# Optimization experiments

Hardware: AMD Instinct MI355X
Metric: run time of the kernel (lower is better)

The kernel has to match this reference:

```python
import jax, jax.numpy as jnp
import numpy as np

B, N, C = 4, 1370, 1024
H, DH = 16, C // 16
N_ROPE = 1369  # patch tokens covered by RoPE (prefix=1 CLS token)


def _rotate_half(x):
    x1, x2 = jnp.split(x, 2, axis=-1)
    return jnp.concatenate([-x2, x1], axis=-1)


def _rope_apply(x, sin, cos):
    return x * cos + _rotate_half(x) * sin


def setup_inputs() -> dict:
    key = jax.random.key(0)
    ks = jax.random.split(key, 7)
    return {
        "x": jax.random.normal(ks[0], (B, N, C), dtype=jnp.float32),
        "sin": jax.random.normal(ks[1], (N_ROPE, DH), dtype=jnp.float32),
        "cos": jax.random.normal(ks[2], (N_ROPE, DH), dtype=jnp.float32),
        "w_qkv": jax.random.normal(ks[3], (C, 3 * C), dtype=jnp.float32) * (C ** -0.5),
        "b_qkv": jax.random.normal(ks[4], (3 * C,), dtype=jnp.float32) * 0.02,
        "w_proj": jax.random.normal(ks[5], (C, C), dtype=jnp.float32) * (C ** -0.5),
        "b_proj": jax.random.normal(ks[6], (C,), dtype=jnp.float32) * 0.02,
    }


def reference(x, sin, cos, w_qkv, b_qkv, w_proj, b_proj):
    b, n, c = x.shape
    # QKV projection -> [3, B, H, N, DH]
    qkv = (x @ w_qkv + b_qkv).reshape(b, n, 3, H, DH).transpose(2, 0, 3, 1, 4)
    q, k, v = qkv[0], qkv[1], qkv[2]
    # RoPE on the last N_ROPE tokens (prefix tokens, e.g. CLS, left untouched)
    prefix = n - sin.shape[-2]
    q = jnp.concatenate([q[:, :, :prefix, :], _rope_apply(q[:, :, prefix:, :], sin, cos)], axis=-2)
    k = jnp.concatenate([k[:, :, :prefix, :], _rope_apply(k[:, :, prefix:, :], sin, cos)], axis=-2)
    # Full attention
    scale = 1.0 / jnp.sqrt(jnp.asarray(DH, dtype=x.dtype))
    attn = jnp.einsum('bhqd,bhkd->bhqk', q, k) * scale
    attn = jax.nn.softmax(attn, axis=-1)
    out = jnp.einsum('bhqk,bhkd->bhqd', attn, v)
    out = out.transpose(0, 2, 1, 3).reshape(b, n, c)
    return out @ w_proj + b_proj
```

## Files before the change

### kernel.cpp

```cpp
#include <hip/hip_runtime.h>
#include <hip/hip_bf16.h>

#define B_ 4
#define N_ 1370
#define C_ 1024
#define H_ 16
#define DH_ 64
#define NR_ 1369
#define M_ (B_*N_)
#define VTS_ 1408
#define ALS 64
#define PLS 72

#define QSCALE 0.1803368801111f

typedef _Float16 f16x8  __attribute__((ext_vector_type(8)));
typedef __bf16   bf16x8 __attribute__((ext_vector_type(8)));
typedef float    f32x4  __attribute__((ext_vector_type(4)));

__device__ __forceinline__ f16x8 ld_frag_h(const unsigned short* p) {
    uint4 u = *(const uint4*)p;
    return __builtin_bit_cast(f16x8, u);
}
__device__ __forceinline__ bf16x8 ld_frag_b(const unsigned short* p) {
    uint4 u = *(const uint4*)p;
    return __builtin_bit_cast(bf16x8, u);
}
__device__ __forceinline__ unsigned short f2h(float f) {
    _Float16 h = (_Float16)f;
    return __builtin_bit_cast(unsigned short, h);
}
__device__ __forceinline__ unsigned short f2bf(float f) {
    __hip_bfloat16 h = __float2bfloat16(f);
    return __builtin_bit_cast(unsigned short, h);
}
__device__ __forceinline__ bf16x8 ones_bf() {
    uint4 u = make_uint4(0x3F803F80u, 0x3F803F80u, 0x3F803F80u, 0x3F803F80u);
    return __builtin_bit_cast(bf16x8, u);
}

__device__ __forceinline__ void load_lds16(const unsigned short* g, unsigned short* l) {
    __builtin_amdgcn_global_load_lds(
        (const __attribute__((address_space(1))) unsigned int*)g,
        (__attribute__((address_space(3))) unsigned int*)l,
        16, 0, 0);
}

#define XBLK 5480
#define WQBLK 768
#define WPBLK 256
__global__ __launch_bounds__(256)
void prep_k(const float* __restrict__ x, unsigned short* __restrict__ xo,
            const float* __restrict__ wq, unsigned short* __restrict__ wqt,
            const float* __restrict__ wp, unsigned short* __restrict__ wpt)
{
    __shared__ unsigned short Th[64][68];
    int bid = blockIdx.x;
    if (bid < XBLK) {
        const int i = bid * 256 + threadIdx.x;
        float4 v = ((const float4*)x)[i];
        ushort4 h;
        h.x = f2h(v.x); h.y = f2h(v.y); h.z = f2h(v.z); h.w = f2h(v.w);
        ((ushort4*)xo)[i] = h;
        return;
    }
    bid -= XBLK;
    const float* w; unsigned short* wt; int Ncol, nb;
    if (bid < WQBLK) { w = wq; wt = wqt; Ncol = 3072; nb = 48; }
    else { bid -= WQBLK; w = wp; wt = wpt; Ncol = 1024; nb = 16; }
    const int tid = threadIdx.x, tx = tid & 15, ty = tid >> 4;
    const int n0 = (bid % nb) * 64, k0 = (bid / nb) * 64;
    #pragma unroll
    for (int i = 0; i < 4; ++i) {
        const int k = ty + i * 16;
        float4 v = *(const float4*)&w[(size_t)(k0 + k) * Ncol + n0 + tx * 4];
        Th[k][tx*4+0] = f2h(v.x); Th[k][tx*4+1] = f2h(v.y);
        Th[k][tx*4+2] = f2h(v.z); Th[k][tx*4+3] = f2h(v.w);
    }
    __syncthreads();
    #pragma unroll
    for (int i = 0; i < 4; ++i) {
        const int n = ty + i * 16;
        ushort4 o;
        o.x = Th[tx*4+0][n]; o.y = Th[tx*4+1][n]; o.z = Th[tx*4+2][n]; o.w = Th[tx*4+3][n];
        *(ushort4*)&wt[(size_t)(n0 + n) * 1024 + k0 + tx * 4] = o;
    }
}

__global__ __launch_bounds__(256)
void transpose_v_k(const unsigned short* __restrict__ v, unsigned short* __restrict__ vt) {
    __shared__ unsigned short Th[64][68];
    const int tid = threadIdx.x, tx = tid & 15, ty = tid >> 4;
    const int bh = blockIdx.y, t0 = blockIdx.x * 64;
    const unsigned short* vp = v + (size_t)bh * N_ * DH_;
    unsigned short* vtp = vt + (size_t)bh * DH_ * VTS_;
    #pragma unroll
    for (int i = 0; i < 4; ++i) {
        const int tok = ty + i * 16;
        const int gtok = t0 + tok;
        ushort4 val;
        if (gtok < N_) val = *(const ushort4*)&vp[(size_t)gtok * DH_ + tx * 4];
        else { val.x = 0; val.y = 0; val.z = 0; val.w = 0; }
        Th[tok][tx*4+0] = val.x; Th[tok][tx*4+1] = val.y;
        Th[tok][tx*4+2] = val.z; Th[tok][tx*4+3] = val.w;
    }
    __syncthreads();
    #pragma unroll
    for (int i = 0; i < 4; ++i) {
        const int d = ty + i * 16;
        ushort4 o;
        o.x = Th[tx*4+0][d]; o.y = Th[tx*4+1][d]; o.z = Th[tx*4+2][d]; o.w = Th[tx*4+3][d];
        *(ushort4*)&vtp[(size_t)d * VTS_ + t0 + tx * 4] = o;
    }
}

__global__ __launch_bounds__(512, 4)
void gemm_qkv8(const unsigned short* __restrict__ A, const unsigned short* __restrict__ Bt,
               const float* __restrict__ bias,
               unsigned short* __restrict__ qb, unsigned short* __restrict__ kb,
               unsigned short* __restrict__ vb,
               const float* __restrict__ sinp, const float* __restrict__ cosp)
{
    __shared__ __align__(16) unsigned short A_s[2][192 * 64];
    __shared__ __align__(16) unsigned short B_s[2][128 * 64];

    const int tid = threadIdx.x;
    const int wave = tid >> 6, lane = tid & 63;
    const int quad = lane >> 4, l16 = lane & 15;
    const int m0 = blockIdx.y * 192, n0 = blockIdx.x * 128;
    const int mwave = (wave >> 1) * 48;
    const int nwave = (wave & 1) * 64;

    const int srow = lane >> 3;
    const int gseg = (lane & 7) ^ srow;

    f32x4 acc[3][4] = {};

    auto stage = [&](int kc, int buf) {
        const int kof = kc * 64;
        #pragma unroll
        for (int i = 0; i < 3; ++i) {
            const int rbase = wave * 24 + i * 8;
            int arow = m0 + rbase + srow;
            if (arow > M_ - 1) arow = M_ - 1;
            load_lds16(A + (size_t)arow * 1024 + kof + gseg * 8, &A_s[buf][rbase * 64]);
        }
        #pragma unroll
        for (int i = 0; i < 2; ++i) {
            const int rbase = wave * 16 + i * 8;
            const int brow = n0 + rbase + srow;
            load_lds16(Bt + (size_t)brow * 1024 + kof + gseg * 8, &B_s[buf][rbase * 64]);
        }
    };

    stage(0, 0);

    for (int kc = 0; kc < 16; ++kc) {
        const int cur = kc & 1;
        __syncthreads();
        if (kc + 1 < 16) stage(kc + 1, cur ^ 1);

        #pragma unroll
        for (int kh = 0; kh < 2; ++kh) {
            const int soff = (((kh * 4 + quad) ^ (l16 & 7)) << 3);
            f16x8 a[3], b[4];
            #pragma unroll
            for (int t = 0; t < 3; ++t)
                a[t] = ld_frag_h(&A_s[cur][(mwave + t * 16 + l16) * 64 + soff]);
            #pragma unroll
            for (int t = 0; t < 4; ++t)
                b[t] = ld_frag_h(&B_s[cur][(nwave + t * 16 + l16) * 64 + soff]);
            #pragma unroll
            for (int i = 0; i < 3; ++i)
                #pragma unroll
                for (int j = 0; j < 4; ++j)
                    acc[i][j] = __builtin_amdgcn_mfma_f32_16x16x32_f16(a[i], b[j], acc[i][j], 0, 0, 0);
        }
    }

    const int nbase = n0 + nwave;
    const int part = nbase >> 10;
    const int h = (nbase & 1023) >> 6;
    #pragma unroll
    for (int i = 0; i < 3; ++i) {
        #pragma unroll
        for (int r = 0; r < 4; ++r) {
            const int gm = m0 + mwave + i * 16 + quad * 4 + r;
            if (gm >= M_) continue;
            const int b = gm / N_;
            const int tok = gm - b * N_;

            float val[4];
            #pragma unroll
            for (int j = 0; j < 4; ++j)
                val[j] = acc[i][j][r] + bias[nbase + j * 16 + l16];

            if (part < 2 && tok >= 1) {
                const float* sp = sinp + (size_t)(tok - 1) * DH_;
                const float* cp = cosp + (size_t)(tok - 1) * DH_;
                const float s0 = sp[l16],      s1 = sp[16 + l16];
                const float s2 = sp[32 + l16], s3 = sp[48 + l16];
                const float c0 = cp[l16],      c1 = cp[16 + l16];
                const float c2 = cp[32 + l16], c3 = cp[48 + l16];
                const float n0v = fmaf(val[0], c0, -val[2] * s0);
                const float n1v = fmaf(val[1], c1, -val[3] * s1);
                const float n2v = fmaf(val[2], c2,  val[0] * s2);
                const float n3v = fmaf(val[3], c3,  val[1] * s3);
                val[0] = n0v; val[1] = n1v; val[2] = n2v; val[3] = n3v;
            }

            const int bh = b * H_ + h;
            #pragma unroll
            for (int j = 0; j < 4; ++j) {
                const int d = j * 16 + l16;
                if (part == 0)      qb[((size_t)bh * N_ + tok) * DH_ + d] = f2h(val[j] * QSCALE);
                else if (part == 1) kb[((size_t)bh * N_ + tok) * DH_ + d] = f2h(val[j]);
                else                vb[((size_t)bh * N_ + tok) * DH_ + d] = f2bf(val[j]);
            }
        }
    }
}

__global__ __launch_bounds__(256)
void gemm_proj2(const unsigned short* __restrict__ A, const unsigned short* __restrict__ Bt,
                const float* __restrict__ bias, float* __restrict__ out)
{
    __shared__ __align__(16) unsigned short A_s[2][64 * 64];
    __shared__ __align__(16) unsigned short B_s[2][128 * 64];

    const int tid = threadIdx.x;
    const int wave = tid >> 6, lane = tid & 63;
    const int quad = lane >> 4, l16 = lane & 15;
    const int m0 = blockIdx.y * 64, n0 = blockIdx.x * 128;
    const int mwave = (wave & 1) * 32, nwave = (wave >> 1) * 64;

    const int srow = lane >> 3;
    const int gseg = (lane & 7) ^ srow;

    f32x4 acc[2][4] = {};

    auto stage = [&](int kc, int buf) {
        const int kof = kc * 64;
        #pragma unroll
        for (int i = 0; i < 2; ++i) {
            const int rbase = wave * 16 + i * 8;
            int arow = m0 + rbase + srow;
            if (arow > M_ - 1) arow = M_ - 1;
            load_lds16(A + (size_t)arow * 1024 + kof + gseg * 8, &A_s[buf][rbase * 64]);
        }
        #pragma unroll
        for (int i = 0; i < 4; ++i) {
            const int rbase = wave * 32 + i * 8;
            const int brow = n0 + rbase + srow;
            load_lds16(Bt + (size_t)brow * 1024 + kof + gseg * 8, &B_s[buf][rbase * 64]);
        }
    };

    stage(0, 0);

    for (int kc = 0; kc < 16; ++kc) {
        const int cur = kc & 1;
        __syncthreads();
        if (kc + 1 < 16) stage(kc + 1, cur ^ 1);

        #pragma unroll
        for (int kh = 0; kh < 2; ++kh) {
            const int soff = (((kh * 4 + quad) ^ (l16 & 7)) << 3);
            f16x8 a[2], b[4];
            #pragma unroll
            for (int t = 0; t < 2; ++t)
                a[t] = ld_frag_h(&A_s[cur][(mwave + t * 16 + l16) * 64 + soff]);
            #pragma unroll
            for (int t = 0; t < 4; ++t)
                b[t] = ld_frag_h(&B_s[cur][(nwave + t * 16 + l16) * 64 + soff]);
            #pragma unroll
            for (int i = 0; i < 2; ++i)
                #pragma unroll
                for (int j = 0; j < 4; ++j)
                    acc[i][j] = __builtin_amdgcn_mfma_f32_16x16x32_f16(a[i], b[j], acc[i][j], 0, 0, 0);
        }
    }

    #pragma unroll
    for (int i = 0; i < 2; ++i) {
        #pragma unroll
        for (int r = 0; r < 4; ++r) {
            const int gm = m0 + mwave + i * 16 + quad * 4 + r;
            if (gm >= M_) continue;
            #pragma unroll
            for (int j = 0; j < 4; ++j) {
                const int gn = n0 + nwave + j * 16 + l16;
                out[(size_t)gm * 1024 + gn] = acc[i][j][r] + bias[gn];
            }
        }
    }
}

__global__ __launch_bounds__(512, 6)
void attn_k(const unsigned short* __restrict__ q, const unsigned short* __restrict__ k,
            const unsigned short* __restrict__ vt, unsigned short* __restrict__ out)
{
    __shared__ __align__(16) unsigned short Ks[2][64 * ALS];
    __shared__ __align__(16) unsigned short Vs[2][64 * ALS];
    __shared__ __align__(16) unsigned short Ps[8 * 16 * PLS];

    const int tid  = threadIdx.x;
    const int wave = tid >> 6, lane = tid & 63;
    const int quad = lane >> 4, l16 = lane & 15;
    const int srow = lane >> 3;
    const int gseg = (lane & 7) ^ srow;

    const int id  = blockIdx.x;
    const int lid = (id & 7) * 88 + (id >> 3);
    const int bh  = lid / 11;
    const int q0  = (lid - bh * 11) * 128;

    const unsigned short* qp  = q  + (size_t)bh * N_ * DH_;
    const unsigned short* kp  = k  + (size_t)bh * N_ * DH_;
    const unsigned short* vtp = vt + (size_t)bh * DH_ * VTS_;

    f16x8 qf[2];
    {
        int qrow = q0 + wave * 16 + l16;
        if (qrow > N_ - 1) qrow = N_ - 1;
        qf[0] = ld_frag_h(qp + (size_t)qrow * DH_ + quad * 8);
        qf[1] = ld_frag_h(qp + (size_t)qrow * DH_ + 32 + quad * 8);
    }

    const bf16x8 onesv = ones_bf();
    f32x4 O[4] = {};
    f32x4 L = {};

    unsigned short* Pw = Ps + wave * 16 * PLS;
    const int so0 = ((quad)     ^ (l16 & 7)) << 3;
    const int so1 = ((4 + quad) ^ (l16 & 7)) << 3;

    auto stage = [&](int ch, int buf) {
        const int k0 = ch * 64;
        const int rbase = wave * 8;
        int krow = k0 + rbase + srow;
        if (krow > N_ - 1) krow = N_ - 1;
        load_lds16(kp + (size_t)krow * DH_ + gseg * 8, &Ks[buf][rbase * ALS]);
        load_lds16(vtp + (size_t)(rbase + srow) * VTS_ + k0 + gseg * 8, &Vs[buf][rbase * ALS]);
    };

    stage(0, 0);

    for (int ch = 0; ch < 22; ++ch) {
        const int k0 = ch * 64;
        const int cur = ch & 1;
        __syncthreads();
        if (ch + 1 < 22) stage(ch + 1, 1 - cur);

        f16x8 kf[4][2];
        #pragma unroll
        for (int t = 0; t < 4; ++t) {
            kf[t][0] = ld_frag_h(&Ks[cur][(t * 16 + l16) * ALS + so0]);
            kf[t][1] = ld_frag_h(&Ks[cur][(t * 16 + l16) * ALS + so1]);
        }
        f32x4 S[4];
        #pragma unroll
        for (int t = 0; t < 4; ++t) {
            f32x4 z = {};
            z = __builtin_amdgcn_mfma_f32_16x16x32_f16(qf[0], kf[t][0], z, 0, 0, 0);
            z = __builtin_amdgcn_mfma_f32_16x16x32_f16(qf[1], kf[t][1], z, 0, 0, 0);
            S[t] = z;
        }
        if (k0 + 64 > N_) {
            #pragma unroll
            for (int t = 0; t < 4; ++t) {
                if (k0 + t * 16 + l16 >= N_) {
                    S[t][0] = -1e30f; S[t][1] = -1e30f;
                    S[t][2] = -1e30f; S[t][3] = -1e30f;
                }
            }
        }

        #pragma unroll
        for (int t = 0; t < 4; ++t) {
            #pragma unroll
            for (int r = 0; r < 4; ++r) {
                const float p = __builtin_amdgcn_exp2f(S[t][r]);
                Pw[(quad * 4 + r) * PLS + t * 16 + l16] = f2bf(p);
            }
        }
        __builtin_amdgcn_wave_barrier();

        bf16x8 pf[2];
        pf[0] = ld_frag_b(&Pw[l16 * PLS + quad * 8]);
        pf[1] = ld_frag_b(&Pw[l16 * PLS + 32 + quad * 8]);

        bf16x8 vf[4][2];
        #pragma unroll
        for (int dt = 0; dt < 4; ++dt) {
            vf[dt][0] = ld_frag_b(&Vs[cur][(dt * 16 + l16) * ALS + so0]);
            vf[dt][1] = ld_frag_b(&Vs[cur][(dt * 16 + l16) * ALS + so1]);
        }
        L = __builtin_amdgcn_mfma_f32_16x16x32_bf16(pf[0], onesv, L, 0, 0, 0);
        L = __builtin_amdgcn_mfma_f32_16x16x32_bf16(pf[1], onesv, L, 0, 0, 0);
        #pragma unroll
        for (int dt = 0; dt < 4; ++dt) {
            O[dt] = __builtin_amdgcn_mfma_f32_16x16x32_bf16(pf[0], vf[dt][0], O[dt], 0, 0, 0);
            O[dt] = __builtin_amdgcn_mfma_f32_16x16x32_bf16(pf[1], vf[dt][1], O[dt], 0, 0, 0);
        }
    }

    const int b = bh >> 4, h = bh & 15;
    #pragma unroll
    for (int r = 0; r < 4; ++r) {
        const int qi = q0 + wave * 16 + quad * 4 + r;
        if (qi < N_) {
            const float inv = 1.0f / L[r];
            unsigned short* op = out + ((size_t)(b * N_ + qi)) * C_ + h * DH_ + l16;
            #pragma unroll
            for (int dt = 0; dt < 4; ++dt) op[dt * 16] = f2h(O[dt][r] * inv);
        }
    }
}

extern "C" void kernel_launch(void* const* d_in, const int* in_sizes, int n_in,
                              void* d_out, int out_size, void* d_ws, size_t ws_size,
                              hipStream_t stream) {
    const float* x      = (const float*)d_in[0];
    const float* sinp   = (const float*)d_in[1];
    const float* cosp   = (const float*)d_in[2];
    const float* w_qkv  = (const float*)d_in[3];
    const float* b_qkv  = (const float*)d_in[4];
    const float* w_proj = (const float*)d_in[5];
    const float* b_proj = (const float*)d_in[6];
    float* out = (float*)d_out;

    unsigned short* p = (unsigned short*)d_ws;
    const size_t xsz  = (size_t)M_ * C_;
    const size_t wqsz = (size_t)3 * C_ * C_;
    const size_t wpsz = (size_t)C_ * C_;
    const size_t hsz  = (size_t)B_ * H_ * N_ * DH_;
    const size_t vtsz = (size_t)B_ * H_ * DH_ * VTS_;
    unsigned short* x_h   = p;            p += xsz;
    unsigned short* wq_t  = p;            p += wqsz;
    unsigned short* wp_t  = p;            p += wpsz;
    unsigned short* q     = p;            p += hsz;
    unsigned short* k     = p;            p += hsz;
    unsigned short* vt    = p;            p += vtsz;
    unsigned short* attnb = p;            p += xsz;
    unsigned short* vb    = attnb;

    prep_k<<<dim3(XBLK + WQBLK + WPBLK), 256, 0, stream>>>(
        x, x_h, w_qkv, wq_t, w_proj, wp_t);

    gemm_qkv8<<<dim3(3 * C_ / 128, (M_ + 191) / 192), 512, 0, stream>>>(
        x_h, wq_t, b_qkv, q, k, vb, sinp, cosp);

    transpose_v_k<<<dim3(VTS_ / 64, B_ * H_), 256, 0, stream>>>(vb, vt);

    attn_k<<<dim3(11 * B_ * H_), 512, 0, stream>>>(q, k, vt, attnb);

    gemm_proj2<<<dim3(C_ / 128, (M_ + 63) / 64), 256, 0, stream>>>(
        attnb, wp_t, b_proj, out);
}
```

Measured before the change: 230.2 us.

## Unify GEMMs into templated 192x128 kernel with XCD-aware block swizzle

Replaces the separate projection GEMM (64x128 tiles, 256 threads) with a templated version of the 512-thread 192x128 QKV GEMM, selecting the epilogue by a MODE parameter. Both GEMMs now launch a 1D grid whose block ids are permuted so consecutive tiles land on the same XCD, improving L2 reuse of A/B panels. The projection gets larger tiles and more operand reuse per block, but only 232 blocks, which may underfill the CUs.

New measurement: 232.9 us. About the same (+1.2%).

```diff
diff --git a/kernel.cpp b/kernel.cpp
--- a/kernel.cpp
+++ b/kernel.cpp
@@ -114,12 +114,13 @@
     }
 }
 
+template<int MODE, int NBLK, int GRID>
 __global__ __launch_bounds__(512, 4)
-void gemm_qkv8(const unsigned short* __restrict__ A, const unsigned short* __restrict__ Bt,
-               const float* __restrict__ bias,
-               unsigned short* __restrict__ qb, unsigned short* __restrict__ kb,
-               unsigned short* __restrict__ vb,
-               const float* __restrict__ sinp, const float* __restrict__ cosp)
+void gemm8(const unsigned short* __restrict__ A, const unsigned short* __restrict__ Bt,
+           const float* __restrict__ bias, float* __restrict__ out,
+           unsigned short* __restrict__ qb, unsigned short* __restrict__ kb,
+           unsigned short* __restrict__ vb,
+           const float* __restrict__ sinp, const float* __restrict__ cosp)
 {
     __shared__ __align__(16) unsigned short A_s[2][192 * 64];
     __shared__ __align__(16) unsigned short B_s[2][128 * 64];
@@ -127,7 +128,12 @@
     const int tid = threadIdx.x;
     const int wave = tid >> 6, lane = tid & 63;
     const int quad = lane >> 4, l16 = lane & 15;
-    const int m0 = blockIdx.y * 192, n0 = blockIdx.x * 128;
+
+    const int id  = blockIdx.x;
+    const int lid = (id & 7) * (GRID / 8) + (id >> 3);
+    const int mblk = lid / NBLK, nblk = lid - mblk * NBLK;
+    const int m0 = mblk * 192, n0 = nblk * 128;
+
     const int mwave = (wave >> 1) * 48;
     const int nwave = (wave & 1) * 64;
 
@@ -178,119 +184,60 @@
         }
     }
 
-    const int nbase = n0 + nwave;
-    const int part = nbase >> 10;
-    const int h = (nbase & 1023) >> 6;
-    #pragma unroll
-    for (int i = 0; i < 3; ++i) {
-        #pragma unroll
-        for (int r = 0; r < 4; ++r) {
-            const int gm = m0 + mwave + i * 16 + quad * 4 + r;
-            if (gm >= M_) continue;
-            const int b = gm / N_;
-            const int tok = gm - b * N_;
-
-            float val[4];
-            #pragma unroll
-            for (int j = 0; j < 4; ++j)
-                val[j] = acc[i][j][r] + bias[nbase + j * 16 + l16];
-
-            if (part < 2 && tok >= 1) {
-                const float* sp = sinp + (size_t)(tok - 1) * DH_;
-                const float* cp = cosp + (size_t)(tok - 1) * DH_;
-                const float s0 = sp[l16],      s1 = sp[16 + l16];
-                const float s2 = sp[32 + l16], s3 = sp[48 + l16];
-                const float c0 = cp[l16],      c1 = cp[16 + l16];
-                const float c2 = cp[32 + l16], c3 = cp[48 + l16];
-                const float n0v = fmaf(val[0], c0, -val[2] * s0);
-                const float n1v = fmaf(val[1], c1, -val[3] * s1);
-                const float n2v = fmaf(val[2], c2,  val[0] * s2);
-                const float n3v = fmaf(val[3], c3,  val[1] * s3);
-                val[0] = n0v; val[1] = n1v; val[2] = n2v; val[3] = n3v;
+    if (MODE == 0) {
+        #pragma unroll
+        for (int i = 0; i < 3; ++i) {
+            #pragma unroll
+            for (int r = 0; r < 4; ++r) {
+                const int gm = m0 + mwave + i * 16 + quad * 4 + r;
+                if (gm >= M_) continue;
+                #pragma unroll
+                for (int j = 0; j < 4; ++j) {
+                    const int gn = n0 + nwave + j * 16 + l16;
+                    out[(size_t)gm * 1024 + gn] = acc[i][j][r] + bias[gn];
+                }
             }
-
-            const int bh = b * H_ + h;
-            #pragma unroll
-            for (int j = 0; j < 4; ++j) {
-                const int d = j * 16 + l16;
-                if (part == 0)      qb[((size_t)bh * N_ + tok) * DH_ + d] = f2h(val[j] * QSCALE);
-                else if (part == 1) kb[((size_t)bh * N_ + tok) * DH_ + d] = f2h(val[j]);
-                else                vb[((size_t)bh * N_ + tok) * DH_ + d] = f2bf(val[j]);
-            }
-        }
-    }
-}
-
-__global__ __launch_bounds__(256)
-void gemm_proj2(const unsigned short* __restrict__ A, const unsigned short* __restrict__ Bt,
-                const float* __restrict__ bias, float* __restrict__ out)
-{
-    __shared__ __align__(16) unsigned short A_s[2][64 * 64];
-    __shared__ __align__(16) unsigned short B_s[2][128 * 64];
-
-    const int tid = threadIdx.x;
-    const int wave = tid >> 6, lane = tid & 63;
-    const int quad = lane >> 4, l16 = lane & 15;
-    const int m0 = blockIdx.y * 64, n0 = blockIdx.x * 128;
-    const int mwave = (wave & 1) * 32, nwave = (wave >> 1) * 64;
-
-    const int srow = lane >> 3;
-    const int gseg = (lane & 7) ^ srow;
-
-    f32x4 acc[2][4] = {};
-
-    auto stage = [&](int kc, int buf) {
-        const int kof = kc * 64;
-        #pragma unroll
-        for (int i = 0; i < 2; ++i) {
-            const int rbase = wave * 16 + i * 8;
-            int arow = m0 + rbase + srow;
-            if (arow > M_ - 1) arow = M_ - 1;
-            load_lds16(A + (size_t)arow * 1024 + kof + gseg * 8, &A_s[buf][rbase * 64]);
-        }
-        #pragma unroll
-        for (int i = 0; i < 4; ++i) {
-            const int rbase = wave * 32 + i * 8;
-            const int brow = n0 + rbase + srow;
-            load_lds16(Bt + (size_t)brow * 1024 + kof + gseg * 8, &B_s[buf][rbase * 64]);
-        }
-    };
-
-    stage(0, 0);
-
-    for (int kc = 0; kc < 16; ++kc) {
-        const int cur = kc & 1;
-        __syncthreads();
-        if (kc + 1 < 16) stage(kc + 1, cur ^ 1);
-
-        #pragma unroll
-        for (int kh = 0; kh < 2; ++kh) {
-            const int soff = (((kh * 4 + quad) ^ (l16 & 7)) << 3);
-            f16x8 a[2], b[4];
-            #pragma unroll
-            for (int t = 0; t < 2; ++t)
-                a[t] = ld_frag_h(&A_s[cur][(mwave + t * 16 + l16) * 64 + soff]);
-            #pragma unroll
-            for (int t = 0; t < 4; ++t)
-                b[t] = ld_frag_h(&B_s[cur][(nwave + t * 16 + l16) * 64 + soff]);
-            #pragma unroll
-            for (int i = 0; i < 2; ++i)
+        }
+    } else {
+        const int nbase = n0 + nwave;
+        const int part = nbase >> 10;
+        const int h = (nbase & 1023) >> 6;
+        #pragma unroll
+        for (int i = 0; i < 3; ++i) {
+            #pragma unroll
+            for (int r = 0; r < 4; ++r) {
+                const int gm = m0 + mwave + i * 16 + quad * 4 + r;
+                if (gm >= M_) continue;
+                const int b = gm / N_;
+                const int tok = gm - b * N_;
+
+                float val[4];
                 #pragma unroll
                 for (int j = 0; j < 4; ++j)
-                    acc[i][j] = __builtin_amdgcn_mfma_f32_16x16x32_f16(a[i], b[j], acc[i][j], 0, 0, 0);
-        }
-    }
-
-    #pragma unroll
-    for (int i = 0; i < 2; ++i) {
-        #pragma unroll
-        for (int r = 0; r < 4; ++r) {
-            const int gm = m0 + mwave + i * 16 + quad * 4 + r;
-            if (gm >= M_) continue;
-            #pragma unroll
-            for (int j = 0; j < 4; ++j) {
-                const int gn = n0 + nwave + j * 16 + l16;
-                out[(size_t)gm * 1024 + gn] = acc[i][j][r] + bias[gn];
+                    val[j] = acc[i][j][r] + bias[nbase + j * 16 + l16];
+
+                if (part < 2 && tok >= 1) {
+                    const float* sp = sinp + (size_t)(tok - 1) * DH_;
+                    const float* cp = cosp + (size_t)(tok - 1) * DH_;
+                    const float s0 = sp[l16],      s1 = sp[16 + l16];
+                    const float s2 = sp[32 + l16], s3 = sp[48 + l16];
+                    const float c0 = cp[l16],      c1 = cp[16 + l16];
+                    const float c2 = cp[32 + l16], c3 = cp[48 + l16];
+                    const float n0v = fmaf(val[0], c0, -val[2] * s0);
+                    const float n1v = fmaf(val[1], c1, -val[3] * s1);
+                    const float n2v = fmaf(val[2], c2,  val[0] * s2);
+                    const float n3v = fmaf(val[3], c3,  val[1] * s3);
+                    val[0] = n0v; val[1] = n1v; val[2] = n2v; val[3] = n3v;
+                }
+
+                const int bh = b * H_ + h;
+                #pragma unroll
+                for (int j = 0; j < 4; ++j) {
+                    const int d = j * 16 + l16;
+                    if (part == 0)      qb[((size_t)bh * N_ + tok) * DH_ + d] = f2h(val[j] * QSCALE);
+                    else if (part == 1) kb[((size_t)bh * N_ + tok) * DH_ + d] = f2h(val[j]);
+                    else                vb[((size_t)bh * N_ + tok) * DH_ + d] = f2bf(val[j]);
+                }
             }
         }
     }
@@ -448,13 +395,13 @@
     prep_k<<<dim3(XBLK + WQBLK + WPBLK), 256, 0, stream>>>(
         x, x_h, w_qkv, wq_t, w_proj, wp_t);
 
-    gemm_qkv8<<<dim3(3 * C_ / 128, (M_ + 191) / 192), 512, 0, stream>>>(
-        x_h, wq_t, b_qkv, q, k, vb, sinp, cosp);
+    gemm8<1, 24, 696><<<dim3(696), 512, 0, stream>>>(
+        x_h, wq_t, b_qkv, nullptr, q, k, vb, sinp, cosp);
 
     transpose_v_k<<<dim3(VTS_ / 64, B_ * H_), 256, 0, stream>>>(vb, vt);
 
     attn_k<<<dim3(11 * B_ * H_), 512, 0, stream>>>(q, k, vt, attnb);
 
-    gemm_proj2<<<dim3(C_ / 128, (M_ + 63) / 64), 256, 0, stream>>>(
-        attnb, wp_t, b_proj, out);
-}
+    gemm8<0, 8, 232><<<dim3(232), 512, 0, stream>>>(
+        attnb, wp_t, b_proj, out, nullptr, nullptr, nullptr, nullptr, nullptr);
+}
```
